# Kernel optimization log

Hardware: AMD Instinct MI355X
Metric: run time of the kernel (lower is better)

## Reference

```python
import jax, jax.numpy as jnp
import numpy as np

EPS = 1e-6
BETA = 0.5
B, T, N = 128, 30, 10000   # batch, BP iterations, n error bits
M, K = 5000, 10            # checks, observables
CHK_W, OBS_W = 6, 50       # row weights of chkmat / obsmat


def _make_supports():
    """Deterministic sparse supports (CSR-style flattened col indices + row ids)."""
    rng = np.random.default_rng(0)
    chk_rows = np.argpartition(rng.random((M, N)), CHK_W, axis=1)[:, :CHK_W]
    obs_rows = np.argpartition(rng.random((K, N)), OBS_W, axis=1)[:, :OBS_W]
    chk_idx = chk_rows.reshape(-1).astype(np.int32)
    chk_seg = np.repeat(np.arange(M, dtype=np.int32), CHK_W)
    obs_idx = obs_rows.reshape(-1).astype(np.int32)
    obs_seg = np.repeat(np.arange(K, dtype=np.int32), OBS_W)
    return chk_idx, chk_seg, obs_idx, obs_seg


def setup_inputs() -> dict:
    key = jax.random.key(0)
    k1, k2, k3 = jax.random.split(key, 3)
    all_llrs = jax.random.normal(k1, (B, T, N), dtype=jnp.float32) * 2.0
    syndromes = jax.random.randint(k2, (B, M), 0, 2, dtype=jnp.int32)
    observables = jax.random.randint(k3, (B, K), 0, 2, dtype=jnp.int32)
    chk_idx, chk_seg, obs_idx, obs_seg = _make_supports()
    return {
        "all_llrs": all_llrs,
        "syndromes": syndromes,
        "observables": observables,
        "chk_idx": jnp.asarray(chk_idx),
        "chk_seg": jnp.asarray(chk_seg),
        "obs_idx": jnp.asarray(obs_idx),
        "obs_seg": jnp.asarray(obs_seg),
    }


def _pred_llr(t, idx, seg, num_seg):
    # t: (B,T,N) tanh(llr/2); gather support cols -> (B,T,E)
    g = t[:, :, idx]
    # segmented product over support entries (tanh rule), segments on axis 0
    p = jax.ops.segment_prod(jnp.moveaxis(g, 2, 0), seg, num_segments=num_seg)  # (S,B,T)
    p = jnp.clip(jnp.moveaxis(p, 0, 2), -1.0 + EPS, 1.0 - EPS)  # (B,T,S)
    return 2.0 * jnp.arctanh(p)


def _bce_with_logits(z, y):
    # stable BCEWithLogits: max(z,0) - z*y + log(1+exp(-|z|)) == logaddexp(0,z) - z*y
    return jnp.logaddexp(0.0, z) - z * y


def reference(all_llrs, syndromes, observables, chk_idx, chk_seg, obs_idx, obs_seg):
    t = jnp.tanh(all_llrs * 0.5)                                   # (B,T,N)
    syn_llr = _pred_llr(t, chk_idx, chk_seg, syndromes.shape[1])    # (B,T,M)
    obs_llr = _pred_llr(t, obs_idx, obs_seg, observables.shape[1])  # (B,T,K)
    y_syn = syndromes.astype(jnp.float32)[:, None, :]
    y_obs = observables.astype(jnp.float32)[:, None, :]
    loss1 = _bce_with_logits(-syn_llr, y_syn).sum(axis=2)           # (B,T)
    loss2 = _bce_with_logits(-obs_llr, y_obs).sum(axis=2)           # (B,T)
    loss = BETA * loss1 + (1.0 - BETA) * loss2
    return loss.mean()
```

## Files before the change

kernel.cpp:

```cpp
#include <hip/hip_runtime.h>

typedef float floatx2 __attribute__((ext_vector_type(2)));

#define B_  128
#define T_  30
#define N_  10000
#define M_  5000
#define K_  10
#define OBS_W_ 50
#define EPS_ 1e-6f
#define LOG2F_ 0.69314718056f
#define BT_  3840
#define CHUNK_ 200
#define SEGW_  (CHUNK_ / 4)
#define NCHK_ (M_/CHUNK_)
#define NB_ 10
#define NPART_ ((NCHK_ + 1) * (BT_ / 256))
#define PART_OFF_ (40u * 1024u * 1024u)

__device__ __forceinline__ float tanh_half(float x) {
    float r = __builtin_amdgcn_rcpf(__expf(x) + 1.f);
    return __builtin_fmaf(-2.f, r, 1.f);
}

__global__ __launch_bounds__(256) void tanh_transpose_fp8(
    const float*   __restrict__ llrs,
    unsigned char* __restrict__ tt)
{
    __shared__ unsigned int lds[64][65];
    const int bt0 = blockIdx.x * 256;
    const int n0  = blockIdx.y * 64;
    const int tid = threadIdx.x;
    const int c4  = tid & 15;
    const int r4b = tid >> 4;

    #pragma unroll
    for (int it = 0; it < 4; ++it) {
        const int r4 = r4b + 16 * it;
        if (n0 + 4 * c4 < N_) {
            float t[4][4];
            #pragma unroll
            for (int j = 0; j < 4; ++j) {
                float4 v = *(const float4*)(llrs +
                            (size_t)(bt0 + 4 * r4 + j) * N_ + n0 + 4 * c4);
                t[j][0] = tanh_half(v.x);
                t[j][1] = tanh_half(v.y);
                t[j][2] = tanh_half(v.z);
                t[j][3] = tanh_half(v.w);
            }
            #pragma unroll
            for (int k = 0; k < 4; ++k) {
                int pk = __builtin_amdgcn_cvt_pk_fp8_f32(t[0][k], t[1][k], 0, false);
                pk     = __builtin_amdgcn_cvt_pk_fp8_f32(t[2][k], t[3][k], pk, true);
                lds[r4][4 * c4 + k] = (unsigned int)pk;
            }
        }
    }
    __syncthreads();

    const int w = tid & 15;
    #pragma unroll
    for (int it = 0; it < 4; ++it) {
        const int col = (tid >> 4) + 16 * it;
        if (n0 + col < N_) {
            uint4 d;
            d.x = lds[4 * w + 0][col];
            d.y = lds[4 * w + 1][col];
            d.z = lds[4 * w + 2][col];
            d.w = lds[4 * w + 3][col];
            *(uint4*)(tt + (size_t)(n0 + col) * BT_ + bt0 + 16 * w) = d;
        }
    }
}

__device__ __forceinline__ void cvt4(unsigned int qv, float* a) {
    floatx2 lo = __builtin_amdgcn_cvt_pk_f32_fp8((int)qv, false);
    floatx2 hi = __builtin_amdgcn_cvt_pk_f32_fp8((int)qv, true);
    a[0] = lo.x; a[1] = lo.y; a[2] = hi.x; a[3] = hi.y;
}

__global__ __launch_bounds__(256) void gather_loss_fp8(
    const unsigned char* __restrict__ tt,
    const int*           __restrict__ syndromes,
    const int*           __restrict__ observables,
    const int*           __restrict__ chk_idx,
    const int*           __restrict__ obs_idx,
    float*               __restrict__ partials)
{
    __shared__ int   sidx[CHUNK_ * 6];
    __shared__ int   ssyn[NB_][CHUNK_];
    __shared__ float red[4];

    const int tid  = threadIdx.x;
    const int lane = tid & 63;
    const int wave = tid >> 6;
    const int r0   = blockIdx.x * 256 + lane * 4;
    const int bA   = r0 / 30;
    const int bB   = (r0 + 3) / 30;
    const int split= (bA + 1) * 30 - r0;
    const int b_lo = (blockIdx.x * 256) / 30;
    const unsigned char* col0 = tt + r0;
    const int y = blockIdx.y;
    float acc = 0.f;

    if (y < NCHK_) {
        const int m0 = y * CHUNK_;
        for (int i = tid; i < CHUNK_ * 6; i += 256)
            sidx[i] = chk_idx[m0 * 6 + i];
        for (int i = tid; i < NB_ * CHUNK_; i += 256) {
            int bi = i / CHUNK_, j = i - bi * CHUNK_;
            int b  = b_lo + bi; if (b > B_ - 1) b = B_ - 1;
            ((int*)ssyn)[i] = syndromes[(size_t)b * M_ + m0 + j];
        }
        __syncthreads();
        const int iA = bA - b_lo, iB = bB - b_lo;

        #pragma unroll 2
        for (int s = wave * SEGW_; s < wave * SEGW_ + SEGW_; ++s) {
            int i0 = sidx[s * 6 + 0], i1 = sidx[s * 6 + 1], i2 = sidx[s * 6 + 2];
            int i3 = sidx[s * 6 + 3], i4 = sidx[s * 6 + 4], i5 = sidx[s * 6 + 5];
            unsigned int q0 = *(const unsigned int*)(col0 + (size_t)i0 * BT_);
            unsigned int q1 = *(const unsigned int*)(col0 + (size_t)i1 * BT_);
            unsigned int q2 = *(const unsigned int*)(col0 + (size_t)i2 * BT_);
            unsigned int q3 = *(const unsigned int*)(col0 + (size_t)i3 * BT_);
            unsigned int q4 = *(const unsigned int*)(col0 + (size_t)i4 * BT_);
            unsigned int q5 = *(const unsigned int*)(col0 + (size_t)i5 * BT_);
            float a[4], b4[4], p[4];
            cvt4(q0, p);  cvt4(q1, a);  cvt4(q2, b4);
            #pragma unroll
            for (int j = 0; j < 4; ++j) p[j] *= a[j] * b4[j];
            cvt4(q3, a);  cvt4(q4, b4);
            #pragma unroll
            for (int j = 0; j < 4; ++j) p[j] *= a[j] * b4[j];
            cvt4(q5, a);
            float sgA = ssyn[iA][s] ? -1.f : 1.f;
            float sgB = ssyn[iB][s] ? -1.f : 1.f;
            #pragma unroll
            for (int j = 0; j < 4; ++j) {
                float sg = (j >= split) ? sgB : sgA;
                float sp = sg * p[j] * a[j];
                sp = fminf(fmaxf(sp, -1.f + EPS_), 1.f - EPS_);
                acc += 1.0f - __log2f(1.f + sp);
            }
        }
    } else {
        for (int k = wave; k < K_; k += 4) {
            const int* oi = obs_idx + k * OBS_W_;
            float p[4] = {1.f, 1.f, 1.f, 1.f};
            #pragma unroll 5
            for (int j2 = 0; j2 < OBS_W_; ++j2) {
                unsigned int qq = *(const unsigned int*)(col0 + (size_t)oi[j2] * BT_);
                float a[4];
                cvt4(qq, a);
                p[0] *= a[0]; p[1] *= a[1]; p[2] *= a[2]; p[3] *= a[3];
            }
            float sgA = observables[(size_t)bA * K_ + k] ? -1.f : 1.f;
            float sgB = observables[(size_t)bB * K_ + k] ? -1.f : 1.f;
            #pragma unroll
            for (int j = 0; j < 4; ++j) {
                float sg = (j >= split) ? sgB : sgA;
                float sp = sg * p[j];
                sp = fminf(fmaxf(sp, -1.f + EPS_), 1.f - EPS_);
                acc += 1.0f - __log2f(1.f + sp);
            }
        }
    }

    #pragma unroll
    for (int off = 32; off > 0; off >>= 1)
        acc += __shfl_down(acc, off, 64);
    if (lane == 0) red[wave] = acc;
    __syncthreads();
    if (tid == 0)
        partials[y * (BT_ / 256) + blockIdx.x] = red[0] + red[1] + red[2] + red[3];
}

__global__ __launch_bounds__(256) void reduce_partials(
    const float* __restrict__ partials, float* __restrict__ out, int out_size)
{
    __shared__ float red[4];
    const int tid  = threadIdx.x;
    const int lane = tid & 63;
    const int wave = tid >> 6;
    float acc = 0.f;
    for (int i = tid; i < NPART_; i += 256) acc += partials[i];
    #pragma unroll
    for (int off = 32; off > 0; off >>= 1)
        acc += __shfl_down(acc, off, 64);
    if (lane == 0) red[wave] = acc;
    __syncthreads();
    if (tid == 0) {
        float s = red[0] + red[1] + red[2] + red[3];
        out[0] = s * (0.5f * LOG2F_ / (float)BT_);
    }
    for (int i = tid + 1; i < out_size; i += 256) out[i] = 0.f;
}

extern "C" void kernel_launch(void* const* d_in, const int* in_sizes, int n_in,
                              void* d_out, int out_size, void* d_ws, size_t ws_size,
                              hipStream_t stream) {
    const float* all_llrs    = (const float*)d_in[0];
    const int*   syndromes   = (const int*)d_in[1];
    const int*   observables = (const int*)d_in[2];
    const int*   chk_idx     = (const int*)d_in[3];
    const int*   obs_idx     = (const int*)d_in[5];
    float*         out = (float*)d_out;
    unsigned char* tt  = (unsigned char*)d_ws;
    float* partials = (float*)((unsigned char*)d_ws + PART_OFF_);

    dim3 g1(BT_ / 256, (N_ + 63) / 64);
    tanh_transpose_fp8<<<g1, 256, 0, stream>>>(all_llrs, tt);

    dim3 g2(BT_ / 256, NCHK_ + 1);
    gather_loss_fp8<<<g2, 256, 0, stream>>>(
        tt, syndromes, observables, chk_idx, obs_idx, partials);

    reduce_partials<<<1, 256, 0, stream>>>(partials, out, out_size);
}
```

Baseline: 264.2 us.

## Rebalance observable blocks across waves and schedule them first in the grid

The observable-loss blocks used to give each wave whole observables, 50 serial gathers each, so waves were unevenly loaded (k=0..9 over 4 waves). Now each wave takes a strided slice of the 50 support positions for all 10 observables, and the partial products are combined through shared memory. The observable blocks also move to blockIdx.y==0 so these long blocks start first instead of forming a tail. The cost is more LDS use (about 40KB extra), which may reduce occupancy of the check blocks too, since they share the kernel.

New measurement: 264.7 us. Within noise of the previous version (+0.2%).

```diff
diff --git a/kernel.cpp b/kernel.cpp
--- a/kernel.cpp
+++ b/kernel.cpp
@@ -90,6 +90,8 @@
     __shared__ int   sidx[CHUNK_ * 6];
     __shared__ int   ssyn[NB_][CHUNK_];
     __shared__ float red[4];
+    __shared__ float opp[4][K_][64][4];
+    __shared__ int   sobs[K_ * OBS_W_];
 
     const int tid  = threadIdx.x;
     const int lane = tid & 63;
@@ -103,8 +105,8 @@
     const int y = blockIdx.y;
     float acc = 0.f;
 
-    if (y < NCHK_) {
-        const int m0 = y * CHUNK_;
+    if (y > 0) {
+        const int m0 = (y - 1) * CHUNK_;
         for (int i = tid; i < CHUNK_ * 6; i += 256)
             sidx[i] = chk_idx[m0 * 6 + i];
         for (int i = tid; i < NB_ * CHUNK_; i += 256) {
@@ -144,16 +146,42 @@
             }
         }
     } else {
+        for (int i = tid; i < K_ * OBS_W_; i += 256) sobs[i] = obs_idx[i];
+        __syncthreads();
+
+        float pp[K_][4];
+        #pragma unroll
+        for (int k = 0; k < K_; ++k) {
+            #pragma unroll
+            for (int j = 0; j < 4; ++j) pp[k][j] = 1.f;
+        }
+
+        #pragma unroll 4
+        for (int t = 0; t < 13; ++t) {
+            const int j2 = wave + 4 * t;
+            if (j2 < OBS_W_) {
+                #pragma unroll
+                for (int k = 0; k < K_; ++k) {
+                    unsigned int qq = *(const unsigned int*)(
+                        col0 + (size_t)sobs[k * OBS_W_ + j2] * BT_);
+                    float a[4];
+                    cvt4(qq, a);
+                    #pragma unroll
+                    for (int j = 0; j < 4; ++j) pp[k][j] *= a[j];
+                }
+            }
+        }
+        #pragma unroll
+        for (int k = 0; k < K_; ++k)
+            *(float4*)&opp[wave][k][lane][0] =
+                make_float4(pp[k][0], pp[k][1], pp[k][2], pp[k][3]);
+        __syncthreads();
         for (int k = wave; k < K_; k += 4) {
-            const int* oi = obs_idx + k * OBS_W_;
-            float p[4] = {1.f, 1.f, 1.f, 1.f};
-            #pragma unroll 5
-            for (int j2 = 0; j2 < OBS_W_; ++j2) {
-                unsigned int qq = *(const unsigned int*)(col0 + (size_t)oi[j2] * BT_);
-                float a[4];
-                cvt4(qq, a);
-                p[0] *= a[0]; p[1] *= a[1]; p[2] *= a[2]; p[3] *= a[3];
-            }
+            float p[4];
+            #pragma unroll
+            for (int j = 0; j < 4; ++j)
+                p[j] = opp[0][k][lane][j] * opp[1][k][lane][j]
+                     * opp[2][k][lane][j] * opp[3][k][lane][j];
             float sgA = observables[(size_t)bA * K_ + k] ? -1.f : 1.f;
             float sgB = observables[(size_t)bB * K_ + k] ? -1.f : 1.f;
             #pragma unroll
```
